# Kernel tuning notes

Hardware: AMD Instinct MI355X
Metric: run time of the kernel (lower is better)

The kernel has to match this reference:

```python
import jax, jax.numpy as jnp
import numpy as np
from jax import lax

OBS_LEN = 8
PRED_LEN = 12
DIM = 128      # hidden_dim
EMB = 64       # embedding_dim
HEADS = 4
MODES = 5
SCENE = 32     # peds per scene
NPED = 8192    # total peds (256 scenes)


def _lin(key, out_d, in_d):
    kw, kb = jax.random.split(key)
    w = jax.random.normal(kw, (out_d, in_d), jnp.float32) / np.sqrt(in_d).astype(np.float32)
    b = jax.random.normal(kb, (out_d,), jnp.float32) * 0.01
    return w, b


def _stack(key, n, out_d, in_d):
    ws, bs = zip(*[_lin(k, out_d, in_d) for k in jax.random.split(key, n)])
    return jnp.stack(ws), jnp.stack(bs)


def setup_inputs() -> dict:
    key = jax.random.key(0)
    ks = jax.random.split(key, 24)
    inp = {}
    inp['obs_traj'] = jax.random.normal(ks[0], (OBS_LEN, NPED, 2), jnp.float32)
    inp['pe_w'], inp['pe_b'] = _lin(ks[1], EMB, 2)
    inp['lstm_wih'], inp['lstm_bih'] = _lin(ks[2], 4 * DIM, EMB)
    inp['lstm_whh'], inp['lstm_bhh'] = _lin(ks[3], 4 * DIM, DIM)
    inp['rp_w1'], inp['rp_b1'] = _lin(ks[4], DIM // 2, 2)
    inp['rp_w2'], inp['rp_b2'] = _lin(ks[5], DIM, DIM // 2)
    inp['wq'], inp['bq'] = _lin(ks[6], DIM, DIM)
    inp['wk'], inp['bk'] = _lin(ks[7], DIM, DIM)
    inp['wv'], inp['bv'] = _lin(ks[8], DIM, DIM)
    inp['wo'], inp['bo'] = _lin(ks[9], DIM, DIM)
    inp['op_w'], inp['op_b'] = _lin(ks[10], DIM, 2 * DIM)
    inp['mp_w1'], inp['mp_b1'] = _lin(ks[11], DIM, 2 * DIM)
    inp['mp_w2'], inp['mp_b2'] = _lin(ks[12], MODES, DIM)
    inp['td_w1'], inp['td_b1'] = _stack(ks[13], MODES, DIM, 2 * DIM)
    inp['td_w2'], inp['td_b2'] = _stack(ks[14], MODES, DIM, DIM)
    inp['td_w3'], inp['td_b3'] = _stack(ks[15], MODES, PRED_LEN * 2, DIM)
    inp['ud_w1'], inp['ud_b1'] = _stack(ks[16], MODES, DIM // 2, 2 * DIM)
    inp['ud_w2'], inp['ud_b2'] = _stack(ks[17], MODES, PRED_LEN * 2, DIM // 2)
    inp['scene_size'] = SCENE
    return inp


def reference(obs_traj, pe_w, pe_b, lstm_wih, lstm_bih, lstm_whh, lstm_bhh,
              rp_w1, rp_b1, rp_w2, rp_b2, wq, bq, wk, bk, wv, bv, wo, bo,
              op_w, op_b, mp_w1, mp_b1, mp_w2, mp_b2,
              td_w1, td_b1, td_w2, td_b2, td_w3, td_b3,
              ud_w1, ud_b1, ud_w2, ud_b2, scene_size):
    obs = jnp.transpose(obs_traj, (1, 0, 2))          # (N, T, 2)
    N = obs.shape[0]
    D = lstm_whh.shape[1]

    # ---- NodeHistoryEncoder: Linear embed + 1-layer LSTM, last hidden ----
    emb = jnp.einsum('ntd,ed->nte', obs, pe_w) + pe_b  # (N, T, EMB)

    def step(carry, x):
        h, c = carry
        g = x @ lstm_wih.T + lstm_bih + h @ lstm_whh.T + lstm_bhh
        i, f, gg, o = jnp.split(g, 4, axis=-1)          # torch gate order i,f,g,o
        c = jax.nn.sigmoid(f) * c + jax.nn.sigmoid(i) * jnp.tanh(gg)
        h = jax.nn.sigmoid(o) * jnp.tanh(c)
        return (h, c), None

    h0 = jnp.zeros((N, D), obs.dtype)
    (node_features, _), _ = lax.scan(step, (h0, h0), jnp.swapaxes(emb, 0, 1))
    last_pos = obs[:, -1, :]                            # (N, 2)

    # ---- EdgeEncoder: per-scene rel-pos-biased multi-head attention ----
    S = scene_size
    B = N // S
    feat = node_features.reshape(B, S, D)
    pos = last_pos.reshape(B, S, 2)
    rel = pos[:, None, :, :] - pos[:, :, None, :]       # [b,i,j] = pos_j - pos_i
    rel_enc = jax.nn.relu(jnp.einsum('bijd,hd->bijh', rel, rp_w1) + rp_b1)
    rel_enc = jnp.einsum('bijh,eh->bije', rel_enc, rp_w2) + rp_b2  # (B,S,S,D)
    kv = feat[:, None, :, :] + rel_enc                  # key == value
    dh = D // HEADS
    q = (feat @ wq.T + bq).reshape(B, S, HEADS, dh)
    kp = (jnp.einsum('bijd,ed->bije', kv, wk) + bk).reshape(B, S, S, HEADS, dh)
    vp = (jnp.einsum('bijd,ed->bije', kv, wv) + bv).reshape(B, S, S, HEADS, dh)
    scores = jnp.einsum('bihd,bijhd->bhij', q, kp) / np.sqrt(dh).astype(np.float32)
    attn = jax.nn.softmax(scores, axis=-1)
    ctx = jnp.einsum('bhij,bijhd->bihd', attn, vp).reshape(B, S, D)
    attn_out = ctx @ wo.T + bo
    edge = (jnp.concatenate([feat, attn_out], axis=-1) @ op_w.T + op_b).reshape(N, D)

    f_all = jnp.concatenate([node_features, edge], axis=-1)  # (N, 2D)

    # ---- GMMDecoder ----
    probs = jax.nn.softmax(jax.nn.relu(f_all @ mp_w1.T + mp_b1) @ mp_w2.T + mp_b2, axis=-1)
    h1 = jax.nn.relu(jnp.einsum('nd,mhd->nmh', f_all, td_w1) + td_b1)    # (N,M,D)
    h2 = jax.nn.relu(jnp.einsum('nmh,mgh->nmg', h1, td_w2) + td_b2)
    traj = (jnp.einsum('nmg,mog->nmo', h2, td_w3) + td_b3).reshape(N, MODES, PRED_LEN, 2)
    u1 = jax.nn.relu(jnp.einsum('nd,mhd->nmh', f_all, ud_w1) + ud_b1)
    sigmas = jax.nn.softplus(jnp.einsum('nmh,moh->nmo', u1, ud_w2) + ud_b2).reshape(N, MODES, PRED_LEN, 2)
    predictions = jnp.cumsum(traj, axis=2) + last_pos[:, None, None, :]
    return predictions, probs
```

## Files before the change

### kernel.cpp

```cpp
#include <hip/hip_runtime.h>
#include <math.h>

typedef __attribute__((ext_vector_type(8))) short short8;
typedef __attribute__((ext_vector_type(4))) float f32x4;

#define NPED 8192

#define B_WHH    0
#define B_WQKV   131072
#define B_WO     229376
#define B_OPW    262144
#define B_MPW1   327680
#define B_TDW1   393216
#define B_TDW2   720896
#define F_WIHE   884736
#define F_BEFF   888832
#define F_WK2    890880
#define F_WV2T   923648
#define F_BQKV   956416
#define A_FEAT   957952
#define A_QKV    3055104
#define A_H1MP   9346560
#define A_H1TD   11443712
#define B_TDW3C  21929472
#define F_TDB3C  21970432

__device__ __forceinline__ float bf2f(ushort u) {
  union { unsigned i; float f; } v; v.i = ((unsigned)u) << 16; return v.f;
}
__device__ __forceinline__ ushort f2bf(float f) {
  union { float f; unsigned i; } v; v.f = f;
  unsigned r = v.i + 0x7fffu + ((v.i >> 16) & 1u);
  return (ushort)(r >> 16);
}

__global__ __launch_bounds__(256) void prep(
    const float* __restrict__ wih, const float* __restrict__ bih, const float* __restrict__ bhh,
    const float* __restrict__ pew, const float* __restrict__ peb,
    const float* __restrict__ wk, const float* __restrict__ wv,
    const float* __restrict__ rpw2, const float* __restrict__ rpb2,
    const float* __restrict__ bq, const float* __restrict__ bk, const float* __restrict__ bv,
    const float* __restrict__ whh, const float* __restrict__ wq, const float* __restrict__ wo,
    const float* __restrict__ opw, const float* __restrict__ mpw1,
    const float* __restrict__ tdw1, const float* __restrict__ tdw2,
    const float* __restrict__ tdw3, const float* __restrict__ tdb3,
    char* __restrict__ wsb) {
  int tid = blockIdx.x * 256 + threadIdx.x;
  float* wihe = (float*)(wsb + F_WIHE);
  float* beff = (float*)(wsb + F_BEFF);
  float* wk2  = (float*)(wsb + F_WK2);
  float* wv2T = (float*)(wsb + F_WV2T);
  float* bqkv = (float*)(wsb + F_BQKV);
  if (tid < 512) {
    int d = tid;
    float s0 = 0.f, s1 = 0.f, sb = 0.f;
    for (int e = 0; e < 64; ++e) {
      float w = wih[d * 64 + e];
      s0 += w * pew[e * 2]; s1 += w * pew[e * 2 + 1]; sb += w * peb[e];
    }
    wihe[d * 2] = s0; wihe[d * 2 + 1] = s1;
    beff[d] = bih[d] + bhh[d] + sb;
  } else if (tid < 8704) {
    int idx = tid - 512; int d = idx >> 6, e = idx & 63;
    float s = 0.f;
    for (int c = 0; c < 128; ++c) s += wk[d * 128 + c] * rpw2[c * 64 + e];
    wk2[idx] = s;
  } else if (tid < 16896) {
    int idx = tid - 8704; int e = idx >> 7, hd = idx & 127;
    float s = 0.f;
    for (int c = 0; c < 128; ++c) s += wv[hd * 128 + c] * rpw2[c * 64 + e];
    wv2T[idx] = s;
  } else if (tid < 17024) {
    int d = tid - 16896;
    float s = bk[d];
    for (int c = 0; c < 128; ++c) s += wk[d * 128 + c] * rpb2[c];
    bqkv[128 + d] = s;
  } else if (tid < 17152) {
    int d = tid - 17024;
    float s = bv[d];
    for (int c = 0; c < 128; ++c) s += wv[d * 128 + c] * rpb2[c];
    bqkv[256 + d] = s;
  } else if (tid < 17280) {
    int d = tid - 17152;
    bqkv[d] = bq[d];
  } else if (tid >= 17408) {
    int i = tid - 17408;
    if (i < 65536) {
      ((ushort*)(wsb + B_WHH))[i] = f2bf(whh[i]);
    } else if (i < 114688) {
      int j = i - 65536; int n = j >> 7, k = j & 127;
      float v = (n < 128) ? wq[n * 128 + k] : (n < 256) ? wk[(n - 128) * 128 + k] : wv[(n - 256) * 128 + k];
      ((ushort*)(wsb + B_WQKV))[j] = f2bf(v);
    } else if (i < 131072) {
      int j = i - 114688; ((ushort*)(wsb + B_WO))[j] = f2bf(wo[j]);
    } else if (i < 163840) {
      int j = i - 131072; ((ushort*)(wsb + B_OPW))[j] = f2bf(opw[j]);
    } else if (i < 196608) {
      int j = i - 163840; ((ushort*)(wsb + B_MPW1))[j] = f2bf(mpw1[j]);
    } else if (i < 360448) {
      int j = i - 196608; ((ushort*)(wsb + B_TDW1))[j] = f2bf(tdw1[j]);
    } else if (i < 442368) {
      int j = i - 360448; ((ushort*)(wsb + B_TDW2))[j] = f2bf(tdw2[j]);
    } else if (i < 462848) {
      int j = i - 442368; int m = j >> 12, r = j & 4095, o = r >> 7, k = r & 127;
      float s = 0.f;
      if (o < 24) {
        int c = o & 1, jj = o >> 1;
        for (int jp = 0; jp <= jj; ++jp) s += tdw3[(m * 24 + jp * 2 + c) * 128 + k];
      }
      ((ushort*)(wsb + B_TDW3C))[j] = f2bf(s);
    } else if (i < 462968) {
      int j = i - 462848; int m = j / 24, o = j % 24;
      int c = o & 1, jj = o >> 1;
      float s = 0.f;
      for (int jp = 0; jp <= jj; ++jp) s += tdb3[m * 24 + jp * 2 + c];
      ((float*)(wsb + F_TDB3C))[j] = s;
    }
  }
}

__global__ __launch_bounds__(512) void lstm_mfma(
    const float* __restrict__ obs, const ushort* __restrict__ whhb,
    const float* __restrict__ wihe, const float* __restrict__ beff,
    ushort* __restrict__ feat) {
  __shared__ ushort Hs[32 * 128];
  __shared__ float obs_s[8][32][2];
  int tid = threadIdx.x;
  int w = tid >> 6, l = tid & 63;
  int lm = l & 15, lg = l >> 4;
  int nb = blockIdx.x * 32;
  {
    int ts = tid >> 6, p = (tid >> 1) & 31, c = tid & 1;
    obs_s[ts][p][c] = obs[ts * (NPED * 2) + (nb + p) * 2 + c];
  }
  for (int i = tid; i < 4096; i += 512) Hs[i] = 0;
  short8 bfr[4][4];
  float wx0[4], wx1[4], be[4];
#pragma unroll
  for (int q = 0; q < 4; ++q) {
    int g = q * 128 + w * 16 + lm;
    wx0[q] = wihe[g * 2]; wx1[q] = wihe[g * 2 + 1]; be[q] = beff[g];
#pragma unroll
    for (int ks = 0; ks < 4; ++ks)
      bfr[q][ks] = *(const short8*)(const void*)&whhb[g * 128 + ks * 32 + lg * 8];
  }
  float cst[2][4] = {};
  __syncthreads();
  for (int ts = 0; ts < 8; ++ts) {
    f32x4 acc[2][4];
#pragma unroll
    for (int mi = 0; mi < 2; ++mi)
#pragma unroll
      for (int r = 0; r < 4; ++r) {
        int p = mi * 16 + lg * 4 + r;
        float ox = obs_s[ts][p][0], oy = obs_s[ts][p][1];
#pragma unroll
        for (int q = 0; q < 4; ++q)
          acc[mi][q][r] = be[q] + wx0[q] * ox + wx1[q] * oy;
      }
#pragma unroll
    for (int ks = 0; ks < 4; ++ks) {
      int p0 = lm, p1 = 16 + lm;
      short8 a0 = *(const short8*)(const void*)&Hs[p0 * 128 + ((ks * 32 + lg * 8) ^ ((p0 & 7) << 3))];
      short8 a1 = *(const short8*)(const void*)&Hs[p1 * 128 + ((ks * 32 + lg * 8) ^ ((p1 & 7) << 3))];
#pragma unroll
      for (int q = 0; q < 4; ++q) {
        acc[0][q] = __builtin_amdgcn_mfma_f32_16x16x32_bf16(a0, bfr[q][ks], acc[0][q], 0, 0, 0);
        acc[1][q] = __builtin_amdgcn_mfma_f32_16x16x32_bf16(a1, bfr[q][ks], acc[1][q], 0, 0, 0);
      }
    }
    __syncthreads();
    int d = w * 16 + lm;
#pragma unroll
    for (int mi = 0; mi < 2; ++mi)
#pragma unroll
      for (int r = 0; r < 4; ++r) {
        int p = mi * 16 + lg * 4 + r;
        float xi = acc[mi][0][r], xf = acc[mi][1][r], xg = acc[mi][2][r], xo = acc[mi][3][r];
        float ig = 1.f / (1.f + __expf(-xi));
        float fg = 1.f / (1.f + __expf(-xf));
        xg = fminf(fmaxf(xg, -30.f), 30.f);
        float eg = __expf(-2.f * xg);
        float gg = (1.f - eg) / (1.f + eg);
        float og = 1.f / (1.f + __expf(-xo));
        float cv = fg * cst[mi][r] + ig * gg;
        cst[mi][r] = cv;
        float cvc = fminf(fmaxf(cv, -30.f), 30.f);
        float ec = __expf(-2.f * cvc);
        float th = (1.f - ec) / (1.f + ec);
        ushort hb = f2bf(og * th);
        Hs[p * 128 + (d ^ ((p & 7) << 3))] = hb;
        if (ts == 7) feat[(size_t)(nb + p) * 128 + d] = hb;
      }
    __syncthreads();
  }
}

template<int NF>
__global__ __launch_bounds__(256) void mfma_gemm(
    const ushort* __restrict__ A1, int lda1, int K1,
    const ushort* __restrict__ A2, int lda2,
    const ushort* __restrict__ Bw, int K,
    const float* __restrict__ bias,
    ushort* __restrict__ out, int ldo, int ooff, int relu,
    int sB, int sBias, int sA1, int sOut) {
  int w = threadIdx.x >> 6, l = threadIdx.x & 63;
  int lm = l & 15, lg = l >> 4;
  int z = blockIdx.z;
  A1 += (size_t)z * sA1;
  Bw += (size_t)z * sB;
  bias += (size_t)z * sBias;
  out += (size_t)z * sOut;
  int row = blockIdx.x * 64 + w * 16 + lm;
  int col0 = blockIdx.y * (NF * 16);
  f32x4 acc[NF];
#pragma unroll
  for (int i = 0; i < NF; ++i) acc[i] = (f32x4){0.f, 0.f, 0.f, 0.f};
  const int nks = K >> 5;
  for (int ks = 0; ks < nks; ++ks) {
    int kb = ks * 32 + lg * 8;
    const ushort* ap = (ks * 32 < K1) ? (A1 + (size_t)row * lda1 + kb)
                                      : (A2 + (size_t)row * lda2 + (kb - K1));
    short8 af = *(const short8*)(const void*)ap;
#pragma unroll
    for (int ni = 0; ni < NF; ++ni) {
      short8 bf = *(const short8*)(const void*)(Bw + (size_t)(col0 + ni * 16 + lm) * K + kb);
      acc[ni] = __builtin_amdgcn_mfma_f32_16x16x32_bf16(af, bf, acc[ni], 0, 0, 0);
    }
  }
  int orow0 = blockIdx.x * 64 + w * 16 + lg * 4;
#pragma unroll
  for (int ni = 0; ni < NF; ++ni) {
    int c = col0 + ni * 16 + lm;
    float bv = bias[c];
#pragma unroll
    for (int r = 0; r < 4; ++r) {
      float v = acc[ni][r] + bv;
      if (relu) v = fmaxf(v, 0.f);
      out[(size_t)(orow0 + r) * ldo + ooff + c] = f2bf(v);
    }
  }
}

__global__ __launch_bounds__(256) void traj_mfma(
    const ushort* __restrict__ TD2, const ushort* __restrict__ w3c,
    const float* __restrict__ b3c, const float* __restrict__ obs,
    float* __restrict__ out) {
  int w = threadIdx.x >> 6, l = threadIdx.x & 63;
  int lm = l & 15, lg = l >> 4;
  int m = blockIdx.y;
  const ushort* A = TD2 + (size_t)m * (NPED * 128);
  const ushort* B = w3c + (size_t)m * 4096;
  int row = blockIdx.x * 64 + w * 16 + lm;
  f32x4 acc[2];
  acc[0] = (f32x4){0.f,0.f,0.f,0.f}; acc[1] = (f32x4){0.f,0.f,0.f,0.f};
#pragma unroll
  for (int ks = 0; ks < 4; ++ks) {
    int kb = ks * 32 + lg * 8;
    short8 af = *(const short8*)(const void*)(A + (size_t)row * 128 + kb);
#pragma unroll
    for (int ni = 0; ni < 2; ++ni) {
      short8 bf = *(const short8*)(const void*)(B + (ni * 16 + lm) * 128 + kb);
      acc[ni] = __builtin_amdgcn_mfma_f32_16x16x32_bf16(af, bf, acc[ni], 0, 0, 0);
    }
  }
  int orow0 = blockIdx.x * 64 + w * 16 + lg * 4;
#pragma unroll
  for (int ni = 0; ni < 2; ++ni) {
    int o = ni * 16 + lm;
    if (o < 24) {
      float bb = b3c[m * 24 + o];
      int c = o & 1;
#pragma unroll
      for (int r = 0; r < 4; ++r) {
        int n = orow0 + r;
        out[(size_t)n * 120 + m * 24 + o] = acc[ni][r] + bb + obs[7 * (NPED * 2) + n * 2 + c];
      }
    }
  }
}

__global__ __launch_bounds__(256) void attn_kernel(
    const float* __restrict__ obs, ushort* QKV,
    const float* __restrict__ wk2, const float* __restrict__ wv2T,
    const float* __restrict__ rpw1, const float* __restrict__ rpb1) {
  __shared__ float renc[4][32][65];
  __shared__ float K0s[32][129];
  __shared__ float Qi[4][128];
  __shared__ float QW[4][4][64];
  __shared__ float att[4][4][32];
  __shared__ float AR[4][4][64];
  __shared__ float posS[32][2];
  __shared__ float posI[4][2];
  int t = threadIdx.x;
  int scene = blockIdx.x >> 3, ic = blockIdx.x & 7;
  int i0 = ic * 4, sbase = scene * 32;

  for (int idx = t; idx < 4096; idx += 256) {
    int j = idx >> 7, d = idx & 127;
    K0s[j][d] = bf2f(QKV[(size_t)(sbase + j) * 384 + 128 + d]);
  }
  for (int idx = t; idx < 512; idx += 256) {
    int ii = idx >> 7, d = idx & 127;
    Qi[ii][d] = bf2f(QKV[(size_t)(sbase + i0 + ii) * 384 + d]);
  }
  if (t < 64) posS[t >> 1][t & 1] = obs[7 * (NPED * 2) + (sbase + (t >> 1)) * 2 + (t & 1)];
  if (t >= 64 && t < 72) {
    int q = t - 64;
    posI[q >> 1][q & 1] = obs[7 * (NPED * 2) + (sbase + i0 + (q >> 1)) * 2 + (q & 1)];
  }
  __syncthreads();
  for (int idx = t; idx < 1024; idx += 256) {
    int ii = idx >> 8, h = (idx >> 6) & 3, e = idx & 63;
    float s = 0.f;
    for (int d = 0; d < 32; ++d) s += Qi[ii][h * 32 + d] * wk2[(h * 32 + d) * 64 + e];
    QW[ii][h][e] = s;
  }
  for (int idx = t; idx < 8192; idx += 256) {
    int ii = idx >> 11, j = (idx >> 6) & 31, e = idx & 63;
    float rx = posS[j][0] - posI[ii][0], ry = posS[j][1] - posI[ii][1];
    renc[ii][j][e] = fmaxf(rpw1[e * 2] * rx + rpw1[e * 2 + 1] * ry + rpb1[e], 0.f);
  }
  __syncthreads();
  for (int idx = t; idx < 512; idx += 256) {
    int ii = idx >> 7, h = (idx >> 5) & 3, j = idx & 31;
    float s = 0.f;
    for (int d = 0; d < 32; ++d) s += Qi[ii][h * 32 + d] * K0s[j][h * 32 + d];
    for (int e = 0; e < 64; ++e) s += QW[ii][h][e] * renc[ii][j][e];
    att[ii][h][j] = s * 0.1767766952966369f;
  }
  __syncthreads();
  {
    int r = t >> 4, lj = t & 15;
    float v0 = att[r >> 2][r & 3][lj], v1 = att[r >> 2][r & 3][lj + 16];
    float mx = fmaxf(v0, v1);
    mx = fmaxf(mx, __shfl_xor(mx, 8, 16));
    mx = fmaxf(mx, __shfl_xor(mx, 4, 16));
    mx = fmaxf(mx, __shfl_xor(mx, 2, 16));
    mx = fmaxf(mx, __shfl_xor(mx, 1, 16));
    float e0 = expf(v0 - mx), e1 = expf(v1 - mx);
    float sm = e0 + e1;
    sm += __shfl_xor(sm, 8, 16);
    sm += __shfl_xor(sm, 4, 16);
    sm += __shfl_xor(sm, 2, 16);
    sm += __shfl_xor(sm, 1, 16);
    float inv = 1.f / sm;
    att[r >> 2][r & 3][lj] = e0 * inv;
    att[r >> 2][r & 3][lj + 16] = e1 * inv;
  }
  __syncthreads();
  for (int idx = t; idx < 1024; idx += 256) {
    int ii = idx >> 8, h = (idx >> 6) & 3, e = idx & 63;
    float s = 0.f;
    for (int j = 0; j < 32; ++j) s += att[ii][h][j] * renc[ii][j][e];
    AR[ii][h][e] = s;
  }
  __syncthreads();
  for (int idx = t; idx < 512; idx += 256) {
    int ii = idx >> 7, hd = idx & 127, h = hd >> 5;
    float s = 0.f;
    for (int j = 0; j < 32; ++j) s += att[ii][h][j] * bf2f(QKV[(size_t)(sbase + j) * 384 + 256 + hd]);
    for (int e = 0; e < 64; ++e) s += AR[ii][h][e] * wv2T[e * 128 + hd];
    QKV[(size_t)(sbase + i0 + ii) * 384 + hd] = f2bf(s);
  }
}

__global__ __launch_bounds__(256) void probs_kernel(
    const ushort* __restrict__ H1, const float* __restrict__ mpw2,
    const float* __restrict__ mpb2, float* __restrict__ out) {
  __shared__ float Hsm[64][129];
  __shared__ float lgt[64][5];
  int t = threadIdx.x, nb = blockIdx.x * 64;
  for (int idx = t; idx < 8192; idx += 256) Hsm[idx >> 7][idx & 127] = bf2f(H1[(size_t)nb * 128 + idx]);
  __syncthreads();
  for (int idx = t; idx < 320; idx += 256) {
    int p = idx / 5, m = idx % 5;
    float s = mpb2[m];
    for (int k = 0; k < 128; ++k) s += Hsm[p][k] * mpw2[m * 128 + k];
    lgt[p][m] = s;
  }
  __syncthreads();
  if (t < 64) {
    float m0 = lgt[t][0];
#pragma unroll
    for (int j = 1; j < 5; ++j) m0 = fmaxf(m0, lgt[t][j]);
    float e[5], s = 0.f;
#pragma unroll
    for (int j = 0; j < 5; ++j) { e[j] = expf(lgt[t][j] - m0); s += e[j]; }
    float inv = 1.f / s;
#pragma unroll
    for (int j = 0; j < 5; ++j) out[983040 + (size_t)(nb + t) * 5 + j] = e[j] * inv;
  }
}

extern "C" void kernel_launch(void* const* d_in, const int* in_sizes, int n_in,
                              void* d_out, int out_size, void* d_ws, size_t ws_size,
                              hipStream_t stream) {
  (void)in_sizes; (void)n_in; (void)out_size; (void)ws_size;
  const float* obs  = (const float*)d_in[0];
  const float* pew  = (const float*)d_in[1];
  const float* peb  = (const float*)d_in[2];
  const float* wih  = (const float*)d_in[3];
  const float* bih  = (const float*)d_in[4];
  const float* whh  = (const float*)d_in[5];
  const float* bhh  = (const float*)d_in[6];
  const float* rpw1 = (const float*)d_in[7];
  const float* rpb1 = (const float*)d_in[8];
  const float* rpw2 = (const float*)d_in[9];
  const float* rpb2 = (const float*)d_in[10];
  const float* wq   = (const float*)d_in[11];
  const float* bq   = (const float*)d_in[12];
  const float* wk   = (const float*)d_in[13];
  const float* bk   = (const float*)d_in[14];
  const float* wv   = (const float*)d_in[15];
  const float* bv   = (const float*)d_in[16];
  const float* wo   = (const float*)d_in[17];
  const float* bo   = (const float*)d_in[18];
  const float* opw  = (const float*)d_in[19];
  const float* opb  = (const float*)d_in[20];
  const float* mpw1 = (const float*)d_in[21];
  const float* mpb1 = (const float*)d_in[22];
  const float* mpw2 = (const float*)d_in[23];
  const float* mpb2 = (const float*)d_in[24];
  const float* tdw1 = (const float*)d_in[25];
  const float* tdb1 = (const float*)d_in[26];
  const float* tdw2 = (const float*)d_in[27];
  const float* tdb2 = (const float*)d_in[28];
  const float* tdw3 = (const float*)d_in[29];
  const float* tdb3 = (const float*)d_in[30];
  char* wsb = (char*)d_ws;
  float* out = (float*)d_out;

  ushort* whhb  = (ushort*)(wsb + B_WHH);
  ushort* wqkvb = (ushort*)(wsb + B_WQKV);
  ushort* wob   = (ushort*)(wsb + B_WO);
  ushort* opwb  = (ushort*)(wsb + B_OPW);
  ushort* mpw1b = (ushort*)(wsb + B_MPW1);
  ushort* tdw1b = (ushort*)(wsb + B_TDW1);
  ushort* tdw2b = (ushort*)(wsb + B_TDW2);
  ushort* tdw3cb= (ushort*)(wsb + B_TDW3C);
  ushort* featb = (ushort*)(wsb + A_FEAT);
  ushort* qkvb  = (ushort*)(wsb + A_QKV);
  ushort* h1mpb = (ushort*)(wsb + A_H1MP);
  ushort* h1tdb = (ushort*)(wsb + A_H1TD);

  prep<<<1877, 256, 0, stream>>>(wih, bih, bhh, pew, peb, wk, wv, rpw2, rpb2,
                                 bq, bk, bv, whh, wq, wo, opw, mpw1, tdw1, tdw2,
                                 tdw3, tdb3, wsb);
  lstm_mfma<<<256, 512, 0, stream>>>(obs, whhb, (float*)(wsb + F_WIHE),
                                     (float*)(wsb + F_BEFF), featb);
  mfma_gemm<4><<<dim3(128, 6, 1), 256, 0, stream>>>(
      featb, 128, 128, featb, 128, wqkvb, 128, (float*)(wsb + F_BQKV),
      qkvb, 384, 0, 0, 0, 0, 0, 0);
  attn_kernel<<<2048, 256, 0, stream>>>(obs, qkvb, (float*)(wsb + F_WK2),
                                        (float*)(wsb + F_WV2T), rpw1, rpb1);
  mfma_gemm<4><<<dim3(128, 2, 1), 256, 0, stream>>>(
      qkvb, 384, 128, qkvb, 384, wob, 128, bo, qkvb, 384, 128, 0, 0, 0, 0, 0);
  mfma_gemm<4><<<dim3(128, 2, 1), 256, 0, stream>>>(
      featb, 128, 128, qkvb + 128, 384, opwb, 256, opb, qkvb, 384, 256, 0, 0, 0, 0, 0);
  mfma_gemm<4><<<dim3(128, 2, 1), 256, 0, stream>>>(
      featb, 128, 128, qkvb + 256, 384, mpw1b, 256, mpb1, h1mpb, 128, 0, 1, 0, 0, 0, 0);
  probs_kernel<<<128, 256, 0, stream>>>(h1mpb, mpw2, mpb2, out);
  mfma_gemm<4><<<dim3(128, 2, 5), 256, 0, stream>>>(
      featb, 128, 128, qkvb + 256, 384, tdw1b, 256, tdb1, h1tdb, 128, 0, 1,
      32768, 128, 0, 1048576);
  mfma_gemm<8><<<dim3(128, 1, 5), 256, 0, stream>>>(
      h1tdb, 128, 128, h1tdb, 128, tdw2b, 128, tdb2, h1tdb, 128, 0, 1,
      16384, 128, 1048576, 1048576);
  traj_mfma<<<dim3(128, 5), 256, 0, stream>>>(h1tdb, tdw3cb, (float*)(wsb + F_TDB3C), obs, out);
}
```

Measured before the change: 315.7 us.

## Move Q·Wk2 projection into MFMA GEMM and pack attention operands as bf16

```diff
diff --git a/kernel.cpp b/kernel.cpp
--- a/kernel.cpp
+++ b/kernel.cpp
@@ -5,6 +5,7 @@
 typedef __attribute__((ext_vector_type(4))) float f32x4;
 
 #define NPED 8192
+#define INVS 0.1767766952966369f
 
 #define B_WHH    0
 #define B_WQKV   131072
@@ -13,20 +14,28 @@
 #define B_MPW1   327680
 #define B_TDW1   393216
 #define B_TDW2   720896
-#define F_WIHE   884736
-#define F_BEFF   888832
-#define F_WK2    890880
-#define F_WV2T   923648
-#define F_BQKV   956416
-#define A_FEAT   957952
-#define A_QKV    3055104
-#define A_H1MP   9346560
-#define A_H1TD   11443712
-#define B_TDW3C  21929472
-#define F_TDB3C  21970432
+#define B_WK2PAD 884736
+#define F_WIHE   950272
+#define F_BEFF   954368
+#define F_WV2T   956416
+#define F_BQKV   989184
+#define F_ZERO   990720
+#define A_FEAT   991744
+#define A_QKV    3088896
+#define A_H1MP   9380352
+#define A_H1TD   11477504
+#define A_QW     11477504
+#define B_TDW3C  21963264
+#define F_TDB3C  22004224
 
 __device__ __forceinline__ float bf2f(ushort u) {
   union { unsigned i; float f; } v; v.i = ((unsigned)u) << 16; return v.f;
+}
+__device__ __forceinline__ float blo(unsigned u) {
+  union { unsigned i; float f; } v; v.i = u << 16; return v.f;
+}
+__device__ __forceinline__ float bhi(unsigned u) {
+  union { unsigned i; float f; } v; v.i = u & 0xffff0000u; return v.f;
 }
 __device__ __forceinline__ ushort f2bf(float f) {
   union { float f; unsigned i; } v; v.f = f;
@@ -48,7 +57,6 @@
   int tid = blockIdx.x * 256 + threadIdx.x;
   float* wihe = (float*)(wsb + F_WIHE);
   float* beff = (float*)(wsb + F_BEFF);
-  float* wk2  = (float*)(wsb + F_WK2);
   float* wv2T = (float*)(wsb + F_WV2T);
   float* bqkv = (float*)(wsb + F_BQKV);
   if (tid < 512) {
@@ -60,36 +68,41 @@
     }
     wihe[d * 2] = s0; wihe[d * 2 + 1] = s1;
     beff[d] = bih[d] + bhh[d] + sb;
-  } else if (tid < 8704) {
-    int idx = tid - 512; int d = idx >> 6, e = idx & 63;
+  } else if (tid < 33280) {
+    int idx = tid - 512; int r = idx >> 7, d = idx & 127;
+    int h = r >> 6, e = r & 63;
     float s = 0.f;
-    for (int c = 0; c < 128; ++c) s += wk[d * 128 + c] * rpw2[c * 64 + e];
-    wk2[idx] = s;
-  } else if (tid < 16896) {
-    int idx = tid - 8704; int e = idx >> 7, hd = idx & 127;
+    if ((d >> 5) == h)
+      for (int c = 0; c < 128; ++c) s += wk[d * 128 + c] * rpw2[c * 64 + e];
+    ((ushort*)(wsb + B_WK2PAD))[idx] = f2bf(s);
+  } else if (tid < 41472) {
+    int idx = tid - 33280; int e = idx >> 7, hd = idx & 127;
     float s = 0.f;
     for (int c = 0; c < 128; ++c) s += wv[hd * 128 + c] * rpw2[c * 64 + e];
     wv2T[idx] = s;
-  } else if (tid < 17024) {
-    int d = tid - 16896;
+  } else if (tid < 41600) {
+    int d = tid - 41472;
     float s = bk[d];
     for (int c = 0; c < 128; ++c) s += wk[d * 128 + c] * rpb2[c];
     bqkv[128 + d] = s;
-  } else if (tid < 17152) {
-    int d = tid - 17024;
+  } else if (tid < 41728) {
+    int d = tid - 41600;
     float s = bv[d];
     for (int c = 0; c < 128; ++c) s += wv[d * 128 + c] * rpb2[c];
     bqkv[256 + d] = s;
-  } else if (tid < 17280) {
-    int d = tid - 17152;
-    bqkv[d] = bq[d];
-  } else if (tid >= 17408) {
-    int i = tid - 17408;
+  } else if (tid < 41856) {
+    int d = tid - 41728;
+    bqkv[d] = bq[d] * INVS;
+  } else if (tid < 42112) {
+    ((float*)(wsb + F_ZERO))[tid - 41856] = 0.f;
+  } else {
+    int i = tid - 42112;
     if (i < 65536) {
       ((ushort*)(wsb + B_WHH))[i] = f2bf(whh[i]);
     } else if (i < 114688) {
       int j = i - 65536; int n = j >> 7, k = j & 127;
-      float v = (n < 128) ? wq[n * 128 + k] : (n < 256) ? wk[(n - 128) * 128 + k] : wv[(n - 256) * 128 + k];
+      float v = (n < 128) ? wq[n * 128 + k] * INVS
+                          : (n < 256) ? wk[(n - 128) * 128 + k] : wv[(n - 256) * 128 + k];
       ((ushort*)(wsb + B_WQKV))[j] = f2bf(v);
     } else if (i < 131072) {
       int j = i - 114688; ((ushort*)(wsb + B_WO))[j] = f2bf(wo[j]);
@@ -281,55 +294,86 @@
 }
 
 __global__ __launch_bounds__(256) void attn_kernel(
-    const float* __restrict__ obs, ushort* QKV,
-    const float* __restrict__ wk2, const float* __restrict__ wv2T,
+    const float* __restrict__ obs, ushort* QKV, const ushort* __restrict__ QW,
+    const float* __restrict__ wv2T,
     const float* __restrict__ rpw1, const float* __restrict__ rpb1) {
-  __shared__ float renc[4][32][65];
-  __shared__ float K0s[32][129];
+  __shared__ ushort K0s[32 * 128];
+  __shared__ ushort V0s[32 * 128];
+  __shared__ ushort renc[4 * 32 * 64];
   __shared__ float Qi[4][128];
-  __shared__ float QW[4][4][64];
+  __shared__ float QWs[4][256];
   __shared__ float att[4][4][32];
   __shared__ float AR[4][4][64];
+  __shared__ float rpx[64], rpy[64], rpb[64];
   __shared__ float posS[32][2];
   __shared__ float posI[4][2];
   int t = threadIdx.x;
-  int scene = blockIdx.x >> 3, ic = blockIdx.x & 7;
+  int scene = blockIdx.x & 255, ic = blockIdx.x >> 8;
   int i0 = ic * 4, sbase = scene * 32;
 
-  for (int idx = t; idx < 4096; idx += 256) {
-    int j = idx >> 7, d = idx & 127;
-    K0s[j][d] = bf2f(QKV[(size_t)(sbase + j) * 384 + 128 + d]);
+  for (int idx = t; idx < 1024; idx += 256) {
+    int arr = idx >> 9, j = (idx >> 4) & 31, c = idx & 15;
+    short8 v = *(const short8*)(const void*)&QKV[(size_t)(sbase + j) * 384 + 128 + arr * 128 + c * 8];
+    ushort* dst = arr ? V0s : K0s;
+    *(short8*)(void*)&dst[j * 128 + (c ^ (j & 7)) * 8] = v;
   }
   for (int idx = t; idx < 512; idx += 256) {
     int ii = idx >> 7, d = idx & 127;
     Qi[ii][d] = bf2f(QKV[(size_t)(sbase + i0 + ii) * 384 + d]);
   }
+  for (int idx = t; idx < 1024; idx += 256) {
+    int ii = idx >> 8, e = idx & 255;
+    QWs[ii][e] = bf2f(QW[(size_t)(sbase + i0 + ii) * 256 + e]);
+  }
   if (t < 64) posS[t >> 1][t & 1] = obs[7 * (NPED * 2) + (sbase + (t >> 1)) * 2 + (t & 1)];
-  if (t >= 64 && t < 72) {
+  else if (t < 72) {
     int q = t - 64;
     posI[q >> 1][q & 1] = obs[7 * (NPED * 2) + (sbase + i0 + (q >> 1)) * 2 + (q & 1)];
-  }
-  __syncthreads();
+  } else if (t >= 128 && t < 192) {
+    int e = t - 128;
+    rpx[e] = rpw1[e * 2]; rpy[e] = rpw1[e * 2 + 1]; rpb[e] = rpb1[e];
+  }
+  __syncthreads();
+
   for (int idx = t; idx < 1024; idx += 256) {
-    int ii = idx >> 8, h = (idx >> 6) & 3, e = idx & 63;
-    float s = 0.f;
-    for (int d = 0; d < 32; ++d) s += Qi[ii][h * 32 + d] * wk2[(h * 32 + d) * 64 + e];
-    QW[ii][h][e] = s;
-  }
-  for (int idx = t; idx < 8192; idx += 256) {
-    int ii = idx >> 11, j = (idx >> 6) & 31, e = idx & 63;
-    float rx = posS[j][0] - posI[ii][0], ry = posS[j][1] - posI[ii][1];
-    renc[ii][j][e] = fmaxf(rpw1[e * 2] * rx + rpw1[e * 2 + 1] * ry + rpb1[e], 0.f);
-  }
-  __syncthreads();
+    int ii = idx >> 8, j = (idx >> 3) & 31, c = idx & 7;
+    float dx = posS[j][0] - posI[ii][0], dy = posS[j][1] - posI[ii][1];
+    short8 pk;
+#pragma unroll
+    for (int r = 0; r < 8; ++r) {
+      int e = c * 8 + r;
+      pk[r] = (short)f2bf(fmaxf(rpx[e] * dx + rpy[e] * dy + rpb[e], 0.f));
+    }
+    *(short8*)(void*)&renc[(ii * 32 + j) * 64 + (c ^ (j & 7)) * 8] = pk;
+  }
+  __syncthreads();
+
   for (int idx = t; idx < 512; idx += 256) {
     int ii = idx >> 7, h = (idx >> 5) & 3, j = idx & 31;
     float s = 0.f;
-    for (int d = 0; d < 32; ++d) s += Qi[ii][h * 32 + d] * K0s[j][h * 32 + d];
-    for (int e = 0; e < 64; ++e) s += QW[ii][h][e] * renc[ii][j][e];
-    att[ii][h][j] = s * 0.1767766952966369f;
-  }
-  __syncthreads();
+#pragma unroll
+    for (int cc = 0; cc < 4; ++cc) {
+      uint4 kv = *(const uint4*)(const void*)&K0s[j * 128 + (((h * 4 + cc) ^ (j & 7)) * 8)];
+      const float4 qa = *(const float4*)&Qi[ii][h * 32 + cc * 8];
+      const float4 qb = *(const float4*)&Qi[ii][h * 32 + cc * 8 + 4];
+      s += blo(kv.x) * qa.x + bhi(kv.x) * qa.y + blo(kv.y) * qa.z + bhi(kv.y) * qa.w;
+      s += blo(kv.z) * qb.x + bhi(kv.z) * qb.y + blo(kv.w) * qb.z + bhi(kv.w) * qb.w;
+    }
+#pragma unroll
+    for (int c = 0; c < 8; ++c) {
+      uint4 rv = *(const uint4*)(const void*)&renc[(ii * 32 + j) * 64 + ((c ^ (j & 7)) * 8)];
+      const float4 wa = *(const float4*)&QWs[ii][c * 8];
+      const float4 wb = *(const float4*)&QWs[ii][c * 8 + 4];
+      (void)wa; (void)wb;
+      const float4 ua = *(const float4*)&QWs[ii][h * 64 + c * 8];
+      const float4 ub = *(const float4*)&QWs[ii][h * 64 + c * 8 + 4];
+      s += blo(rv.x) * ua.x + bhi(rv.x) * ua.y + blo(rv.y) * ua.z + bhi(rv.y) * ua.w;
+      s += blo(rv.z) * ub.x + bhi(rv.z) * ub.y + blo(rv.w) * ub.z + bhi(rv.w) * ub.w;
+    }
+    att[ii][h][j] = s;
+  }
+  __syncthreads();
+
   {
     int r = t >> 4, lj = t & 15;
     float v0 = att[r >> 2][r & 3][lj], v1 = att[r >> 2][r & 3][lj + 16];
@@ -349,19 +393,49 @@
     att[r >> 2][r & 3][lj + 16] = e1 * inv;
   }
   __syncthreads();
-  for (int idx = t; idx < 1024; idx += 256) {
-    int ii = idx >> 8, h = (idx >> 6) & 3, e = idx & 63;
-    float s = 0.f;
-    for (int j = 0; j < 32; ++j) s += att[ii][h][j] * renc[ii][j][e];
-    AR[ii][h][e] = s;
-  }
-  __syncthreads();
-  for (int idx = t; idx < 512; idx += 256) {
-    int ii = idx >> 7, hd = idx & 127, h = hd >> 5;
-    float s = 0.f;
-    for (int j = 0; j < 32; ++j) s += att[ii][h][j] * bf2f(QKV[(size_t)(sbase + j) * 384 + 256 + hd]);
-    for (int e = 0; e < 64; ++e) s += AR[ii][h][e] * wv2T[e * 128 + hd];
-    QKV[(size_t)(sbase + i0 + ii) * 384 + hd] = f2bf(s);
+
+  {
+    int ii = t >> 6, h = (t >> 4) & 3, e4 = t & 15;
+    int c = e4 >> 1, off = (e4 & 1) * 4;
+    float a0 = 0.f, a1 = 0.f, a2 = 0.f, a3 = 0.f;
+    for (int j = 0; j < 32; ++j) {
+      float av = att[ii][h][j];
+      uint2 rv = *(const uint2*)(const void*)&renc[(ii * 32 + j) * 64 + ((c ^ (j & 7)) * 8) + off];
+      a0 += av * blo(rv.x); a1 += av * bhi(rv.x);
+      a2 += av * blo(rv.y); a3 += av * bhi(rv.y);
+    }
+    *(float4*)&AR[ii][h][e4 * 4] = make_float4(a0, a1, a2, a3);
+  }
+  __syncthreads();
+
+  {
+    int ii = t >> 6, l = t & 63;
+    int h5 = l >> 5, hd4 = l & 31;
+    int hd = hd4 * 4, h = hd >> 5;
+    float c0 = 0.f, c1 = 0.f, c2 = 0.f, c3 = 0.f;
+    int cch = hd >> 3, offh = hd & 7;
+    for (int j = h5 * 16; j < h5 * 16 + 16; ++j) {
+      float av = att[ii][h][j];
+      uint2 vv = *(const uint2*)(const void*)&V0s[j * 128 + ((cch ^ (j & 7)) * 8) + offh];
+      c0 += av * blo(vv.x); c1 += av * bhi(vv.x);
+      c2 += av * blo(vv.y); c3 += av * bhi(vv.y);
+    }
+    for (int e4 = h5 * 8; e4 < h5 * 8 + 8; ++e4) {
+      const float4 ar = *(const float4*)&AR[ii][h][e4 * 4];
+#pragma unroll
+      for (int r = 0; r < 4; ++r) {
+        const float4 wv = *(const float4*)&wv2T[(e4 * 4 + r) * 128 + hd];
+        float a = (r == 0) ? ar.x : (r == 1) ? ar.y : (r == 2) ? ar.z : ar.w;
+        c0 += a * wv.x; c1 += a * wv.y; c2 += a * wv.z; c3 += a * wv.w;
+      }
+    }
+    c0 += __shfl_xor(c0, 32); c1 += __shfl_xor(c1, 32);
+    c2 += __shfl_xor(c2, 32); c3 += __shfl_xor(c3, 32);
+    if (h5 == 0) {
+      ushort4 o;
+      o.x = f2bf(c0); o.y = f2bf(c1); o.z = f2bf(c2); o.w = f2bf(c3);
+      *(ushort4*)(void*)&QKV[(size_t)(sbase + i0 + ii) * 384 + hd] = o;
+    }
   }
 }
 
@@ -431,20 +505,22 @@
   char* wsb = (char*)d_ws;
   float* out = (float*)d_out;
 
-  ushort* whhb  = (ushort*)(wsb + B_WHH);
-  ushort* wqkvb = (ushort*)(wsb + B_WQKV);
-  ushort* wob   = (ushort*)(wsb + B_WO);
-  ushort* opwb  = (ushort*)(wsb + B_OPW);
-  ushort* mpw1b = (ushort*)(wsb + B_MPW1);
-  ushort* tdw1b = (ushort*)(wsb + B_TDW1);
-  ushort* tdw2b = (ushort*)(wsb + B_TDW2);
-  ushort* tdw3cb= (ushort*)(wsb + B_TDW3C);
-  ushort* featb = (ushort*)(wsb + A_FEAT);
-  ushort* qkvb  = (ushort*)(wsb + A_QKV);
-  ushort* h1mpb = (ushort*)(wsb + A_H1MP);
-  ushort* h1tdb = (ushort*)(wsb + A_H1TD);
-
-  prep<<<1877, 256, 0, stream>>>(wih, bih, bhh, pew, peb, wk, wv, rpw2, rpb2,
+  ushort* whhb   = (ushort*)(wsb + B_WHH);
+  ushort* wqkvb  = (ushort*)(wsb + B_WQKV);
+  ushort* wob    = (ushort*)(wsb + B_WO);
+  ushort* opwb   = (ushort*)(wsb + B_OPW);
+  ushort* mpw1b  = (ushort*)(wsb + B_MPW1);
+  ushort* tdw1b  = (ushort*)(wsb + B_TDW1);
+  ushort* tdw2b  = (ushort*)(wsb + B_TDW2);
+  ushort* wk2pb  = (ushort*)(wsb + B_WK2PAD);
+  ushort* tdw3cb = (ushort*)(wsb + B_TDW3C);
+  ushort* featb  = (ushort*)(wsb + A_FEAT);
+  ushort* qkvb   = (ushort*)(wsb + A_QKV);
+  ushort* qwb    = (ushort*)(wsb + A_QW);
+  ushort* h1mpb  = (ushort*)(wsb + A_H1MP);
+  ushort* h1tdb  = (ushort*)(wsb + A_H1TD);
+
+  prep<<<1973, 256, 0, stream>>>(wih, bih, bhh, pew, peb, wk, wv, rpw2, rpb2,
                                  bq, bk, bv, whh, wq, wo, opw, mpw1, tdw1, tdw2,
                                  tdw3, tdb3, wsb);
   lstm_mfma<<<256, 512, 0, stream>>>(obs, whhb, (float*)(wsb + F_WIHE),
@@ -452,8 +528,10 @@
   mfma_gemm<4><<<dim3(128, 6, 1), 256, 0, stream>>>(
       featb, 128, 128, featb, 128, wqkvb, 128, (float*)(wsb + F_BQKV),
       qkvb, 384, 0, 0, 0, 0, 0, 0);
-  attn_kernel<<<2048, 256, 0, stream>>>(obs, qkvb, (float*)(wsb + F_WK2),
-                                        (float*)(wsb + F_WV2T), rpw1, rpb1);
+  mfma_gemm<4><<<dim3(128, 4, 1), 256, 0, stream>>>(
+      qkvb, 384, 128, qkvb, 384, wk2pb, 128, (float*)(wsb + F_ZERO),
+      qwb, 256, 0, 0, 0, 0, 0, 0);
+  attn_kernel<<<2048, 256, 0, stream>>>(obs, qkvb, qwb, (float*)(wsb + F_WV2T), rpw1, rpb1);
   mfma_gemm<4><<<dim3(128, 2, 1), 256, 0, stream>>>(
       qkvb, 384, 128, qkvb, 384, wob, 128, bo, qkvb, 384, 128, 0, 0, 0, 0, 0);
   mfma_gemm<4><<<dim3(128, 2, 1), 256, 0, stream>>>(
```

Measured after the change: 297.3 us. -5.8%, faster.
